# Performance work log

Hardware: AMD Instinct MI355X
Metric: run time of the kernel (lower is better)

Reference implementation:

```python
import jax, jax.numpy as jnp
import numpy as np
from jax import lax

K = 7          # local attention kernel size
DIL = 2        # dilation
PAD = 6        # padding -> same spatial size
BN_EPS = 1e-5


def setup_inputs() -> dict:
    key = jax.random.key(0)
    ks = jax.random.split(key, 4)
    B, C, H, W = 16, 256, 56, 56
    x = jax.random.normal(ks[0], (B, C, H, W), dtype=jnp.float32)
    # conv weights scaled for stable activations
    w1 = jax.random.normal(ks[1], (128, C, K, K), dtype=jnp.float32) * 0.02
    b1 = jnp.zeros((128,), dtype=jnp.float32)
    w2 = jax.random.normal(ks[2], (49, 128, 1, 1), dtype=jnp.float32) * 0.05
    b2 = jnp.zeros((49,), dtype=jnp.float32)
    gamma = jnp.ones((49,), dtype=jnp.float32)
    beta = jnp.zeros((49,), dtype=jnp.float32)
    running_mean = jnp.zeros((49,), dtype=jnp.float32)
    running_var = jnp.ones((49,), dtype=jnp.float32)
    return {"x": x, "w1": w1, "b1": b1, "w2": w2, "b2": b2,
            "gamma": gamma, "beta": beta,
            "running_mean": running_mean, "running_var": running_var}


def _picanet_l(x, w1, b1, w2, b2, gamma, beta, running_mean, running_var):
    B, C, H, W = x.shape
    # conv1: 7x7, dilation 2, padding 6 (same size)
    k = lax.conv_general_dilated(
        x, w1, window_strides=(1, 1), padding=((PAD, PAD), (PAD, PAD)),
        rhs_dilation=(DIL, DIL),
        dimension_numbers=("NCHW", "OIHW", "NCHW"))
    k = jax.nn.relu(k + b1[None, :, None, None])
    # conv2: 1x1 -> 49 channels
    k = jnp.einsum("bchw,oc->bohw", k, w2[:, :, 0, 0]) + b2[None, :, None, None]
    # BatchNorm (eval-style, running stats), then relu + softmax over the 49 taps
    inv = gamma * lax.rsqrt(running_var + BN_EPS)
    k = (k - running_mean[None, :, None, None]) * inv[None, :, None, None] + beta[None, :, None, None]
    k = jax.nn.relu(k)
    attn = jax.nn.softmax(k, axis=1)  # [B, 49, H, W]
    # unfold-gather + weighted sum, expressed as 49 shifted slices of the
    # zero-padded input (matches F.unfold(x, 7, dilation=2, padding=6)).
    xpad = jnp.pad(x, ((0, 0), (0, 0), (PAD, PAD), (PAD, PAD)))
    out = jnp.zeros_like(x)
    for i in range(K):
        for j in range(K):
            tap = xpad[:, :, DIL * i: DIL * i + H, DIL * j: DIL * j + W]  # [B,C,H,W]
            out = out + tap * attn[:, i * K + j][:, None]
    return out


def reference(x, w1, b1, w2, b2, gamma, beta, running_mean, running_var):
    return _picanet_l(x, w1, b1, w2, b2, gamma, beta, running_mean, running_var)
```

## Files before the change

kernel.cpp:

```cpp
#include <hip/hip_runtime.h>

typedef _Float16 f16;
typedef __attribute__((__ext_vector_type__(2))) _Float16 f16x2;
typedef __attribute__((__ext_vector_type__(4))) _Float16 f16x4;
typedef __attribute__((__ext_vector_type__(8))) _Float16 f16x8;
typedef __attribute__((__ext_vector_type__(4))) float f32x4;

#define GLDS16(g, l) __builtin_amdgcn_global_load_lds( \
    (const __attribute__((address_space(1))) void*)(g), \
    (__attribute__((address_space(3))) void*)(l), 16, 0, 0)


__global__ __launch_bounds__(256) void prep(
    const float* __restrict__ x, const float* __restrict__ w1,
    f16* __restrict__ xpad, f16* __restrict__ w1h) {
  const int blk = blockIdx.x;
  const int tid = threadIdx.x;
  if (blk < 896) {
    __shared__ f16 t16[56][258];
    const int h = blk % 56, b = blk / 56;
    const float* xp = x + (size_t)b * 256 * 3136 + h * 56;
    for (int f = tid; f < 256 * 56; f += 256) {
      int c = f / 56, w = f % 56;
      t16[w][c] = (f16)xp[(size_t)c * 3136 + w];
    }
    __syncthreads();
    f16* op = xpad + (((size_t)(b * 68) + h + 6) * 68 + 6) * 256;
    for (int g = tid; g < 56 * 32; g += 256) {
      int w = g >> 5, c0 = (g & 31) * 8;
      *(f16x8*)(op + (size_t)w * 256 + c0) = *(const f16x8*)&t16[w][c0];
    }
  } else if (blk < 896 + 2976) {
    const int i = (blk - 896) * 256 + tid;
    uint4* xp4 = (uint4*)xpad;
    int idx4;
    if (i < 417792) {
      int u = i % 2176;
      int row12 = i / 2176;
      int b = row12 / 12, r12 = row12 % 12;
      int r = (r12 < 6) ? r12 : r12 + 56;
      idx4 = (b * 68 + r) * 2176 + u;
    } else {
      int j = i - 417792;
      int u = j % 192;
      int run = j / 192;
      int side = run & 1;
      int br = run >> 1;
      int r = br % 56 + 6, b = br / 56;
      idx4 = (b * 68 + r) * 2176 + (side ? 62 * 32 : 0) + u;
    }
    xp4[idx4] = make_uint4(0u, 0u, 0u, 0u);
  } else {
    const int idx = (blk - 3872) * 256 + tid;
    const int co = idx >> 8, c = idx & 255;
    const int half = c >> 7, cc = (c >> 5) & 3, q = (c >> 3) & 3, e = c & 7;
    const int f = co >> 4, l15 = co & 15;
    const size_t base =
        ((((size_t)(half * 4 + cc) * 8 + f) * 64 + q * 16 + l15) * 8 + e);
    const float* src = w1 + ((size_t)co * 256 + c) * 49;
#pragma unroll 7
    for (int ij = 0; ij < 49; ++ij)
      w1h[base + (size_t)ij * 32768] = (f16)src[ij];
  }
}

__global__ __launch_bounds__(256, 2) void conv1_gemm(
    const f16* __restrict__ xpad, const f16* __restrict__ w1h,
    f16* __restrict__ kbuf) {
  __shared__ f16 strip[16 * 68 * 32];

  const int tid = threadIdx.x;
  const int wid = tid >> 6, lane = tid & 63;
  const int pphys = blockIdx.x;
  const int bid = (pphys & 7) * 56 + (pphys >> 3);
  const int half = bid & 1;
  const int sid = bid >> 1;
  const int b = sid / 14;
  const int h0 = (sid % 14) * 4;

  const int l15 = lane & 15;
  const int q = lane >> 4;
  const int qb = (l15 >> 1) & 3;

  const int mbase = (wid >> 1) * 7;
  const int nbase = (wid & 1) * 4;

  int arow_off[7];
#pragma unroll
  for (int mm = 0; mm < 7; ++mm) {
    int p = (mbase + mm) * 16 + l15;
    int rw = p / 56;
    int w = p - 56 * rw;
    arow_off[mm] = (rw * 68 + w) * 64;
  }

  const char* xg = (const char*)xpad +
                   ((size_t)(b * 68 + h0)) * (68 * 512) + half * 256;
  const char* wB = (const char*)w1h;
  char* Ss = (char*)strip;

  const int half4 = half * 4;
  auto loadB = [&](int cc, int ij, int nn) -> f16x8 {
    int off = (((ij * 8 + half4 + cc) * 8 + nbase + nn) * 64 + lane) * 16;
    return *(const f16x8*)(wB + off);
  };

  f32x4 acc[7][4] = {};
  f16x8 pb0 = loadB(0, 0, 0), pb1 = loadB(0, 0, 1);
  f16x8 pb2 = loadB(0, 0, 2), pb3 = loadB(0, 0, 3);

  for (int cc = 0; cc < 4; ++cc) {
    const int chb = cc * 64;
    __syncthreads();
#pragma unroll
    for (int rr = 0; rr < 17; ++rr) {
      int s = rr * 256 + tid;
      int r = (int)((unsigned)s / 272u);
      int rem = s - r * 272;
      int col = rem >> 2, q4 = rem & 3;
      int qq = q4 ^ ((col >> 1) & 3);
      GLDS16(xg + (size_t)r * (68 * 512) + col * 512 + chb + qq * 16,
             Ss + (rr * 256 + wid * 64) * 16);
    }
    __syncthreads();

#pragma unroll 7
    for (int ij = 0; ij < 49; ++ij) {
      f16x8 b0 = pb0, b1 = pb1, b2 = pb2, b3 = pb3;
      int nij = ij + 1, ncc = cc;
      if (nij == 49) { nij = 0; ++ncc; }
      if (ncc < 4) {
        pb0 = loadB(ncc, nij, 0);
        pb1 = loadB(ncc, nij, 1);
        pb2 = loadB(ncc, nij, 2);
        pb3 = loadB(ncc, nij, 3);
      }
      const int i = (int)((unsigned)ij / 7u);
      const int j = ij - 7 * i;
      const int base_off = i * 8704 + j * 128 + ((q ^ ((qb + j) & 3)) << 4);
      f16x8 a0 = *(const f16x8*)(Ss + arow_off[0] + base_off);
#pragma unroll
      for (int mm = 0; mm < 7; ++mm) {
        f16x8 an = a0;
        if (mm < 6) an = *(const f16x8*)(Ss + arow_off[mm + 1] + base_off);
        acc[mm][0] = __builtin_amdgcn_mfma_f32_16x16x32_f16(a0, b0,
                                                            acc[mm][0], 0, 0, 0);
        acc[mm][1] = __builtin_amdgcn_mfma_f32_16x16x32_f16(a0, b1,
                                                            acc[mm][1], 0, 0, 0);
        acc[mm][2] = __builtin_amdgcn_mfma_f32_16x16x32_f16(a0, b2,
                                                            acc[mm][2], 0, 0, 0);
        acc[mm][3] = __builtin_amdgcn_mfma_f32_16x16x32_f16(a0, b3,
                                                            acc[mm][3], 0, 0, 0);
        a0 = an;
      }
    }
  }

  f16* kh = kbuf + (size_t)half * (50176 * 128);
  const int pbase = (b * 56 + h0) * 56;
#pragma unroll
  for (int mm = 0; mm < 7; ++mm) {
#pragma unroll
    for (int nn = 0; nn < 4; ++nn) {
      const int co = (nbase + nn) * 16 + l15;
#pragma unroll
      for (int r = 0; r < 4; ++r) {
        int p = (mbase + mm) * 16 + q * 4 + r;
        int rw = p / 56;
        int w = p - 56 * rw;
        kh[(size_t)(pbase + rw * 56 + w) * 128 + co] = (f16)acc[mm][nn][r];
      }
    }
  }
}

__global__ __launch_bounds__(128) void conv2_bn_softmax(
    const f16* __restrict__ kbuf, const float* __restrict__ b1,
    const float* __restrict__ w2, const float* __restrict__ b2,
    const float* __restrict__ gamma, const float* __restrict__ beta,
    const float* __restrict__ rmean, const float* __restrict__ rvar,
    float* __restrict__ attn) {
  __shared__ f16 w2s[49 * 128];
  __shared__ float b1s[128];
  __shared__ float outs[128 * 49];
  for (int i = threadIdx.x; i < 49 * 128; i += 128) w2s[i] = (f16)w2[i];
  if (threadIdx.x < 128) b1s[threadIdx.x] = b1[threadIdx.x];
  __syncthreads();
  const int p = blockIdx.x * 128 + threadIdx.x;
  float acc[49];
#pragma unroll
  for (int o = 0; o < 49; ++o) acc[o] = 0.f;
  const f16x8* ka = (const f16x8*)(kbuf + (size_t)p * 128);
  const f16x8* kb = (const f16x8*)(kbuf + (size_t)50176 * 128 + (size_t)p * 128);
  for (int u = 0; u < 16; ++u) {
    f16x8 va = ka[u], vb = kb[u];
    f16x2 kvh[4];
#pragma unroll
    for (int j = 0; j < 4; ++j) {
      float s0 = (float)va[2 * j] + (float)vb[2 * j] + b1s[u * 8 + 2 * j];
      float s1 =
          (float)va[2 * j + 1] + (float)vb[2 * j + 1] + b1s[u * 8 + 2 * j + 1];
      s0 = s0 > 0.f ? s0 : 0.f;
      s1 = s1 > 0.f ? s1 : 0.f;
      kvh[j] = f16x2{(f16)s0, (f16)s1};
    }
#pragma unroll
    for (int o = 0; o < 49; ++o) {
      f16x8 wv = *(const f16x8*)(w2s + o * 128 + u * 8);
#if __has_builtin(__builtin_amdgcn_fdot2)
      acc[o] = __builtin_amdgcn_fdot2(kvh[0], f16x2{wv[0], wv[1]}, acc[o], false);
      acc[o] = __builtin_amdgcn_fdot2(kvh[1], f16x2{wv[2], wv[3]}, acc[o], false);
      acc[o] = __builtin_amdgcn_fdot2(kvh[2], f16x2{wv[4], wv[5]}, acc[o], false);
      acc[o] = __builtin_amdgcn_fdot2(kvh[3], f16x2{wv[6], wv[7]}, acc[o], false);
#else
#pragma unroll
      for (int j = 0; j < 4; ++j)
        acc[o] += (float)kvh[j][0] * (float)wv[2 * j] +
                  (float)kvh[j][1] * (float)wv[2 * j + 1];
#endif
    }
  }
  float mx = -1e30f;
#pragma unroll
  for (int o = 0; o < 49; ++o) {
    float s = acc[o] + b2[o];
    float inv = gamma[o] * rsqrtf(rvar[o] + 1e-5f);
    s = (s - rmean[o]) * inv + beta[o];
    s = s > 0.f ? s : 0.f;
    acc[o] = s;
    mx = fmaxf(mx, s);
  }
  float sum = 0.f;
#pragma unroll
  for (int o = 0; o < 49; ++o) {
    float e = __expf(acc[o] - mx);
    acc[o] = e;
    sum += e;
  }
  const float rinv = 1.f / sum;
  float* orow = outs + threadIdx.x * 49;
#pragma unroll
  for (int o = 0; o < 49; ++o) orow[o] = acc[o] * rinv;
  __syncthreads();
  float* ab = attn + (size_t)blockIdx.x * (128 * 49);
  for (int i = threadIdx.x; i < 128 * 49; i += 128) ab[i] = outs[i];
}

__global__ __launch_bounds__(896, 1) void aggregate2(
    const f16* __restrict__ xpad, const float* __restrict__ attn,
    float* __restrict__ out) {
  __shared__ float t[256][57];
  const int pp = blockIdx.x;
  const int bh = (pp & 7) * 112 + (pp >> 3);
  const int h = bh % 56, b = bh / 56;
  const int tid = threadIdx.x;
  const int wid = tid >> 6, lane = tid & 63;
  const int q = (wid < 7) ? wid * 8 : (wid - 7) * 8 + 1;

  int ap[4];
#pragma unroll
  for (int p = 0; p < 4; ++p) ap[p] = ((b * 56 + h) * 56 + q + 2 * p) * 49;

  float acc[4][4] = {};
  const f16* rowb = xpad + ((size_t)(b * 68 + h) * 68 + q) * 256 + 4 * lane;

  for (int i = 0; i < 7; ++i) {
    const f16* rb = rowb + (size_t)(2 * i * 68) * 256;
#pragma unroll
    for (int tt = 0; tt < 10; ++tt) {
      f16x4 xv = *(const f16x4*)(rb + tt * 512);
      float xf[4];
#pragma unroll
      for (int k = 0; k < 4; ++k) xf[k] = (float)xv[k];
#pragma unroll
      for (int p = 0; p < 4; ++p) {
        const int j = tt - p;
        if (j >= 0 && j < 7) {
          const float a = attn[ap[p] + i * 7 + j];
#pragma unroll
          for (int k = 0; k < 4; ++k) acc[p][k] = fmaf(a, xf[k], acc[p][k]);
        }
      }
    }
  }

#pragma unroll
  for (int p = 0; p < 4; ++p)
#pragma unroll
    for (int k = 0; k < 4; ++k) t[4 * lane + k][q + 2 * p] = acc[p][k];
  __syncthreads();
  float* ob = out + ((size_t)b * 256 * 56 + h) * 56;
  for (int f = tid; f < 256 * 56; f += 896) {
    int c = f / 56, w = f % 56;
    ob[(size_t)c * 3136 + w] = t[c][w];
  }
}

extern "C" void kernel_launch(void* const* d_in, const int* in_sizes, int n_in,
                              void* d_out, int out_size, void* d_ws,
                              size_t ws_size, hipStream_t stream) {
  const float* x = (const float*)d_in[0];
  const float* w1 = (const float*)d_in[1];
  const float* b1 = (const float*)d_in[2];
  const float* w2 = (const float*)d_in[3];
  const float* b2 = (const float*)d_in[4];
  const float* gamma = (const float*)d_in[5];
  const float* beta = (const float*)d_in[6];
  const float* rmean = (const float*)d_in[7];
  const float* rvar = (const float*)d_in[8];
  float* out = (float*)d_out;

  char* ws = (char*)d_ws;
  f16* xpad = (f16*)ws;
  f16* w1h = (f16*)(ws + 37879808);
  f16* kbuf = (f16*)(ws + 41091072);
  float* attn = (float*)(ws + 66781184);

  hipLaunchKernelGGL(prep, dim3(4000), dim3(256), 0, stream, x, w1, xpad, w1h);
  hipLaunchKernelGGL(conv1_gemm, dim3(448), dim3(256), 0, stream, xpad, w1h,
                     kbuf);
  hipLaunchKernelGGL(conv2_bn_softmax, dim3(392), dim3(128), 0, stream, kbuf,
                     b1, w2, b2, gamma, beta, rmean, rvar, attn);
  hipLaunchKernelGGL(aggregate2, dim3(896), dim3(896), 0, stream, xpad, attn,
                     out);
}
```

Measured before the change: 257.3 us.

## Fuse conv2+BN+softmax into aggregation kernel, keep attention in LDS

The separate conv2/BN/softmax kernel is merged into the aggregation kernel. Each block computes the 1x1 conv, BN and ReLU for its 56 positions into shared memory and does the softmax with wave shuffles, so the attention tensor never goes to global memory and one launch is dropped. Two smaller changes come with it: prep block roles are reordered so the zero-fill runs first, and conv1 A-fragment loads are no longer prefetched one step ahead. The fused kernel needs more LDS and adds syncs, and each block recomputes weights staging.

```diff
diff --git a/kernel.cpp b/kernel.cpp
--- a/kernel.cpp
+++ b/kernel.cpp
@@ -16,22 +16,8 @@
     f16* __restrict__ xpad, f16* __restrict__ w1h) {
   const int blk = blockIdx.x;
   const int tid = threadIdx.x;
-  if (blk < 896) {
-    __shared__ f16 t16[56][258];
-    const int h = blk % 56, b = blk / 56;
-    const float* xp = x + (size_t)b * 256 * 3136 + h * 56;
-    for (int f = tid; f < 256 * 56; f += 256) {
-      int c = f / 56, w = f % 56;
-      t16[w][c] = (f16)xp[(size_t)c * 3136 + w];
-    }
-    __syncthreads();
-    f16* op = xpad + (((size_t)(b * 68) + h + 6) * 68 + 6) * 256;
-    for (int g = tid; g < 56 * 32; g += 256) {
-      int w = g >> 5, c0 = (g & 31) * 8;
-      *(f16x8*)(op + (size_t)w * 256 + c0) = *(const f16x8*)&t16[w][c0];
-    }
-  } else if (blk < 896 + 2976) {
-    const int i = (blk - 896) * 256 + tid;
+  if (blk < 2976) {
+    const int i = blk * 256 + tid;
     uint4* xp4 = (uint4*)xpad;
     int idx4;
     if (i < 417792) {
@@ -50,6 +36,21 @@
       idx4 = (b * 68 + r) * 2176 + (side ? 62 * 32 : 0) + u;
     }
     xp4[idx4] = make_uint4(0u, 0u, 0u, 0u);
+  } else if (blk < 2976 + 896) {
+    __shared__ f16 t16[56][258];
+    const int bh = blk - 2976;
+    const int h = bh % 56, b = bh / 56;
+    const float* xp = x + (size_t)b * 256 * 3136 + h * 56;
+    for (int f = tid; f < 256 * 56; f += 256) {
+      int c = f / 56, w = f % 56;
+      t16[w][c] = (f16)xp[(size_t)c * 3136 + w];
+    }
+    __syncthreads();
+    f16* op = xpad + (((size_t)(b * 68) + h + 6) * 68 + 6) * 256;
+    for (int g = tid; g < 56 * 32; g += 256) {
+      int w = g >> 5, c0 = (g & 31) * 8;
+      *(f16x8*)(op + (size_t)w * 256 + c0) = *(const f16x8*)&t16[w][c0];
+    }
   } else {
     const int idx = (blk - 3872) * 256 + tid;
     const int co = idx >> 8, c = idx & 255;
@@ -138,20 +139,17 @@
       const int i = (int)((unsigned)ij / 7u);
       const int j = ij - 7 * i;
       const int base_off = i * 8704 + j * 128 + ((q ^ ((qb + j) & 3)) << 4);
-      f16x8 a0 = *(const f16x8*)(Ss + arow_off[0] + base_off);
 #pragma unroll
       for (int mm = 0; mm < 7; ++mm) {
-        f16x8 an = a0;
-        if (mm < 6) an = *(const f16x8*)(Ss + arow_off[mm + 1] + base_off);
-        acc[mm][0] = __builtin_amdgcn_mfma_f32_16x16x32_f16(a0, b0,
+        f16x8 a = *(const f16x8*)(Ss + arow_off[mm] + base_off);
+        acc[mm][0] = __builtin_amdgcn_mfma_f32_16x16x32_f16(a, b0,
                                                             acc[mm][0], 0, 0, 0);
-        acc[mm][1] = __builtin_amdgcn_mfma_f32_16x16x32_f16(a0, b1,
+        acc[mm][1] = __builtin_amdgcn_mfma_f32_16x16x32_f16(a, b1,
                                                             acc[mm][1], 0, 0, 0);
-        acc[mm][2] = __builtin_amdgcn_mfma_f32_16x16x32_f16(a0, b2,
+        acc[mm][2] = __builtin_amdgcn_mfma_f32_16x16x32_f16(a, b2,
                                                             acc[mm][2], 0, 0, 0);
-        acc[mm][3] = __builtin_amdgcn_mfma_f32_16x16x32_f16(a0, b3,
+        acc[mm][3] = __builtin_amdgcn_mfma_f32_16x16x32_f16(a, b3,
                                                             acc[mm][3], 0, 0, 0);
-        a0 = an;
       }
     }
   }
@@ -174,92 +172,103 @@
   }
 }
 
-__global__ __launch_bounds__(128) void conv2_bn_softmax(
+__global__ __launch_bounds__(896, 1) void agg_fused(
     const f16* __restrict__ kbuf, const float* __restrict__ b1,
     const float* __restrict__ w2, const float* __restrict__ b2,
     const float* __restrict__ gamma, const float* __restrict__ beta,
     const float* __restrict__ rmean, const float* __restrict__ rvar,
-    float* __restrict__ attn) {
-  __shared__ f16 w2s[49 * 128];
-  __shared__ float b1s[128];
-  __shared__ float outs[128 * 49];
-  for (int i = threadIdx.x; i < 49 * 128; i += 128) w2s[i] = (f16)w2[i];
-  if (threadIdx.x < 128) b1s[threadIdx.x] = b1[threadIdx.x];
-  __syncthreads();
-  const int p = blockIdx.x * 128 + threadIdx.x;
-  float acc[49];
-#pragma unroll
-  for (int o = 0; o < 49; ++o) acc[o] = 0.f;
-  const f16x8* ka = (const f16x8*)(kbuf + (size_t)p * 128);
-  const f16x8* kb = (const f16x8*)(kbuf + (size_t)50176 * 128 + (size_t)p * 128);
-  for (int u = 0; u < 16; ++u) {
-    f16x8 va = ka[u], vb = kb[u];
-    f16x2 kvh[4];
-#pragma unroll
-    for (int j = 0; j < 4; ++j) {
-      float s0 = (float)va[2 * j] + (float)vb[2 * j] + b1s[u * 8 + 2 * j];
-      float s1 =
-          (float)va[2 * j + 1] + (float)vb[2 * j + 1] + b1s[u * 8 + 2 * j + 1];
-      s0 = s0 > 0.f ? s0 : 0.f;
-      s1 = s1 > 0.f ? s1 : 0.f;
-      kvh[j] = f16x2{(f16)s0, (f16)s1};
-    }
-#pragma unroll
-    for (int o = 0; o < 49; ++o) {
-      f16x8 wv = *(const f16x8*)(w2s + o * 128 + u * 8);
-#if __has_builtin(__builtin_amdgcn_fdot2)
-      acc[o] = __builtin_amdgcn_fdot2(kvh[0], f16x2{wv[0], wv[1]}, acc[o], false);
-      acc[o] = __builtin_amdgcn_fdot2(kvh[1], f16x2{wv[2], wv[3]}, acc[o], false);
-      acc[o] = __builtin_amdgcn_fdot2(kvh[2], f16x2{wv[4], wv[5]}, acc[o], false);
-      acc[o] = __builtin_amdgcn_fdot2(kvh[3], f16x2{wv[6], wv[7]}, acc[o], false);
-#else
-#pragma unroll
-      for (int j = 0; j < 4; ++j)
-        acc[o] += (float)kvh[j][0] * (float)wv[2 * j] +
-                  (float)kvh[j][1] * (float)wv[2 * j + 1];
-#endif
-    }
-  }
-  float mx = -1e30f;
-#pragma unroll
-  for (int o = 0; o < 49; ++o) {
-    float s = acc[o] + b2[o];
-    float inv = gamma[o] * rsqrtf(rvar[o] + 1e-5f);
-    s = (s - rmean[o]) * inv + beta[o];
-    s = s > 0.f ? s : 0.f;
-    acc[o] = s;
-    mx = fmaxf(mx, s);
-  }
-  float sum = 0.f;
-#pragma unroll
-  for (int o = 0; o < 49; ++o) {
-    float e = __expf(acc[o] - mx);
-    acc[o] = e;
-    sum += e;
-  }
-  const float rinv = 1.f / sum;
-  float* orow = outs + threadIdx.x * 49;
-#pragma unroll
-  for (int o = 0; o < 49; ++o) orow[o] = acc[o] * rinv;
-  __syncthreads();
-  float* ab = attn + (size_t)blockIdx.x * (128 * 49);
-  for (int i = threadIdx.x; i < 128 * 49; i += 128) ab[i] = outs[i];
-}
-
-__global__ __launch_bounds__(896, 1) void aggregate2(
-    const f16* __restrict__ xpad, const float* __restrict__ attn,
-    float* __restrict__ out) {
-  __shared__ float t[256][57];
+    const f16* __restrict__ xpad, float* __restrict__ out) {
+  __shared__ char smem[58368];
+  f16* w2s = (f16*)smem;
+  f16* ks = (f16*)(smem + 13056);
+  float* attnl = (float*)(smem + 28288);
+  float* b1s = (float*)(smem + 39936);
+  float* bninv = (float*)(smem + 40448);
+  float* bnsh = (float*)(smem + 40656);
+  float(*t)[57] = (float(*)[57])smem;
+
   const int pp = blockIdx.x;
   const int bh = (pp & 7) * 112 + (pp >> 3);
   const int h = bh % 56, b = bh / 56;
   const int tid = threadIdx.x;
   const int wid = tid >> 6, lane = tid & 63;
+
+  for (int i = tid; i < 49 * 128; i += 896)
+    w2s[(i >> 7) * 132 + (i & 127)] = (f16)w2[i];
+  if (tid < 128) b1s[tid] = b1[tid];
+  if (tid >= 128 && tid < 177) {
+    int o = tid - 128;
+    float inv = gamma[o] * rsqrtf(rvar[o] + 1e-5f);
+    bninv[o] = inv;
+    bnsh[o] = (b2[o] - rmean[o]) * inv + beta[o];
+  }
+  __syncthreads();
+
+  const int pos1 = tid >> 4, og = tid & 15;
+  const size_t row = ((size_t)bh) * 56 + pos1;
+  {
+    f16x8 va = *(const f16x8*)(kbuf + row * 128 + og * 8);
+    f16x8 vb = *(const f16x8*)(kbuf + (size_t)50176 * 128 + row * 128 + og * 8);
+    f16x8 s;
+#pragma unroll
+    for (int j = 0; j < 8; ++j) {
+      float v = (float)va[j] + (float)vb[j] + b1s[og * 8 + j];
+      s[j] = (f16)(v > 0.f ? v : 0.f);
+    }
+    *(f16x8*)(ks + pos1 * 136 + og * 8) = s;
+  }
+  __syncthreads();
+
+  {
+    f16x8 kc[16];
+#pragma unroll
+    for (int j = 0; j < 16; ++j)
+      kc[j] = *(const f16x8*)(ks + pos1 * 136 + j * 8);
+    const int nout = (og == 0) ? 4 : 3;
+    for (int oi = 0; oi < nout; ++oi) {
+      const int o = (oi == 3) ? 48 : og + oi * 16;
+      float acc = 0.f;
+#pragma unroll
+      for (int j = 0; j < 16; ++j) {
+        f16x8 wv = *(const f16x8*)(w2s + o * 132 + j * 8);
+#if __has_builtin(__builtin_amdgcn_fdot2)
+        acc = __builtin_amdgcn_fdot2(f16x2{kc[j][0], kc[j][1]},
+                                     f16x2{wv[0], wv[1]}, acc, false);
+        acc = __builtin_amdgcn_fdot2(f16x2{kc[j][2], kc[j][3]},
+                                     f16x2{wv[2], wv[3]}, acc, false);
+        acc = __builtin_amdgcn_fdot2(f16x2{kc[j][4], kc[j][5]},
+                                     f16x2{wv[4], wv[5]}, acc, false);
+        acc = __builtin_amdgcn_fdot2(f16x2{kc[j][6], kc[j][7]},
+                                     f16x2{wv[6], wv[7]}, acc, false);
+#else
+#pragma unroll
+        for (int e = 0; e < 8; ++e) acc += (float)kc[j][e] * (float)wv[e];
+#endif
+      }
+      float v = fmaf(acc, bninv[o], bnsh[o]);
+      attnl[pos1 * 52 + o] = v > 0.f ? v : 0.f;
+    }
+  }
+  __syncthreads();
+
   const int q = (wid < 7) ? wid * 8 : (wid - 7) * 8 + 1;
+#pragma unroll
+  for (int p = 0; p < 4; ++p) {
+    const int pos = q + 2 * p;
+    float raw = (lane < 49) ? attnl[pos * 52 + lane] : -1e30f;
+    float m = raw;
+#pragma unroll
+    for (int d = 32; d >= 1; d >>= 1) m = fmaxf(m, __shfl_xor(m, d));
+    float e = (lane < 49) ? __expf(raw - m) : 0.f;
+    float s = e;
+#pragma unroll
+    for (int d = 32; d >= 1; d >>= 1) s += __shfl_xor(s, d);
+    if (lane < 49) attnl[pos * 52 + lane] = e / s;
+  }
 
   int ap[4];
 #pragma unroll
-  for (int p = 0; p < 4; ++p) ap[p] = ((b * 56 + h) * 56 + q + 2 * p) * 49;
+  for (int p = 0; p < 4; ++p) ap[p] = (q + 2 * p) * 52;
 
   float acc[4][4] = {};
   const f16* rowb = xpad + ((size_t)(b * 68 + h) * 68 + q) * 256 + 4 * lane;
@@ -276,7 +285,7 @@
       for (int p = 0; p < 4; ++p) {
         const int j = tt - p;
         if (j >= 0 && j < 7) {
-          const float a = attn[ap[p] + i * 7 + j];
+          const float a = attnl[ap[p] + i * 7 + j];
 #pragma unroll
           for (int k = 0; k < 4; ++k) acc[p][k] = fmaf(a, xf[k], acc[p][k]);
         }
@@ -284,6 +293,7 @@
     }
   }
 
+  __syncthreads();
 #pragma unroll
   for (int p = 0; p < 4; ++p)
 #pragma unroll
@@ -314,13 +324,10 @@
   f16* xpad = (f16*)ws;
   f16* w1h = (f16*)(ws + 37879808);
   f16* kbuf = (f16*)(ws + 41091072);
-  float* attn = (float*)(ws + 66781184);
 
   hipLaunchKernelGGL(prep, dim3(4000), dim3(256), 0, stream, x, w1, xpad, w1h);
   hipLaunchKernelGGL(conv1_gemm, dim3(448), dim3(256), 0, stream, xpad, w1h,
                      kbuf);
-  hipLaunchKernelGGL(conv2_bn_softmax, dim3(392), dim3(128), 0, stream, kbuf,
-                     b1, w2, b2, gamma, beta, rmean, rvar, attn);
-  hipLaunchKernelGGL(aggregate2, dim3(896), dim3(896), 0, stream, xpad, attn,
-                     out);
+  hipLaunchKernelGGL(agg_fused, dim3(896), dim3(896), 0, stream, kbuf, b1, w2,
+                     b2, gamma, beta, rmean, rvar, xpad, out);
 }
```

Measured after the change: 304.9 us. 1.18x slower.
